# Kernel tuning notes

Hardware: AMD Instinct MI355X
Metric: run time of the kernel (lower is better)

Reference implementation:

```python
import jax, jax.numpy as jnp
import numpy as np

HIDDEN = 1024
HEADS = 16
HEAD_DIM = HIDDEN // HEADS
RANK = 256
B, S = 4, 2048


def setup_inputs() -> dict:
    key = jax.random.key(0)
    ks = jax.random.split(key, 10)
    sc_in = 1.0 / np.sqrt(HIDDEN)
    sc_r = 1.0 / np.sqrt(RANK)
    inp = {"hidden_states": jax.random.normal(ks[0], (B, S, HIDDEN), dtype=jnp.float32)}
    names = ["q", "k", "v"]
    for i, n in enumerate(names):
        inp[f"{n}A"] = jax.random.normal(ks[1 + 3 * i], (HIDDEN, RANK), dtype=jnp.float32) * sc_in
        inp[f"{n}B"] = jax.random.normal(ks[2 + 3 * i], (RANK, HIDDEN), dtype=jnp.float32) * sc_r
        inp[f"{n}b"] = jnp.zeros((HIDDEN,), dtype=jnp.float32)
    return inp


def _split_heads(x):
    # [B,S,H*D] -> [B,H,S,D]
    Bh, Sh, _ = x.shape
    return x.reshape(Bh, Sh, HEADS, HEAD_DIM).transpose(0, 2, 1, 3)


def reference(hidden_states, qA, qB, qb, kA, kB, kb, vA, vB, vb):
    # Low-rank projections: x @ A @ B + b (factorized linear)
    q = hidden_states @ qA @ qB + qb
    k = hidden_states @ kA @ kB + kb
    v = hidden_states @ vA @ vB + vb
    q = _split_heads(q)  # [B,H,S,D]
    k = _split_heads(k)
    v = _split_heads(v)
    scores = jnp.einsum("bhqd,bhkd->bhqk", q, k) / np.sqrt(HEAD_DIM)
    probs = jax.nn.softmax(scores, axis=-1)  # dropout is identity at inference
    ctx = jnp.einsum("bhqk,bhkd->bhqd", probs, v)
    ctx = ctx.transpose(0, 2, 1, 3).reshape(hidden_states.shape[0], hidden_states.shape[1], HIDDEN)
    return ctx
```

## Files before the change

kernel.cpp:

```cpp
#include <hip/hip_runtime.h>


typedef unsigned short u16;
typedef unsigned int   u32;
typedef __attribute__((ext_vector_type(4)))  float    f32x4;
typedef __attribute__((ext_vector_type(16))) float    f32x16;
typedef __attribute__((ext_vector_type(8)))  short    short8;
typedef __attribute__((ext_vector_type(8)))  _Float16 half8;
typedef __attribute__((ext_vector_type(4)))  u16      u16x4;

#define HID 1024
#define R_  256
#define S_  2048
#define B_  4
#define H_  16
#define D_  64
#define M_  (B_ * S_)

#define BM 128
#define BN 64
#define BK 64

#define KVB 64
#define NT  (S_ / KVB)
#define SCL 0.18033688011112f
#define MSHIFT 8.0f

__device__ __forceinline__ u16 f2h(float f) {
    _Float16 h = (_Float16)f;
    return __builtin_bit_cast(u16, h);
}
__device__ __forceinline__ u32 pkrtz(float a, float b) {
    auto r = __builtin_amdgcn_cvt_pkrtz(a, b);
    return __builtin_bit_cast(u32, r);
}

__device__ __forceinline__ f32x4 mfma16(short8 a, short8 b, f32x4 c) {
    return __builtin_amdgcn_mfma_f32_16x16x32_f16(
        __builtin_bit_cast(half8, a), __builtin_bit_cast(half8, b), c, 0, 0, 0);
}
__device__ __forceinline__ f32x16 mfma32(short8 a, short8 b, f32x16 c) {
    return __builtin_amdgcn_mfma_f32_32x32x16_f16(
        __builtin_bit_cast(half8, a), __builtin_bit_cast(half8, b), c, 0, 0, 0);
}

__device__ __forceinline__ void gload16(const u16* g, u16* l) {
    __builtin_amdgcn_global_load_lds(
        (__attribute__((address_space(1))) const void*)g,
        (__attribute__((address_space(3))) void*)l,
        16, 0, 0);
}

#if defined(__has_builtin)
#if __has_builtin(__builtin_amdgcn_permlane32_swap)
#define HAVE_PLSWAP 1
#endif
#endif
__device__ __forceinline__ void plswap(u32 x, u32 y, u32& lo, u32& hi) {
#ifdef HAVE_PLSWAP
    typedef __attribute__((ext_vector_type(2))) unsigned uv2;
    uv2 r = __builtin_amdgcn_permlane32_swap(x, y, false, false);
    lo = r.x; hi = r.y;
#else
    u32 ty = (u32)__shfl_xor((int)y, 32);
    u32 tx = (u32)__shfl_xor((int)x, 32);
    int h = (threadIdx.x & 63) >> 5;
    lo = h ? ty : x;
    hi = h ? y : tx;
#endif
}

__global__ __launch_bounds__(256) void prep_kernel(
    const float* __restrict__ hs, u16* __restrict__ hsb,
    const float* __restrict__ qA, const float* __restrict__ kA, const float* __restrict__ vA,
    const float* __restrict__ qB, const float* __restrict__ kB, const float* __restrict__ vB,
    u16* __restrict__ At, u16* __restrict__ Bt) {
    int bx = blockIdx.x;
    if (bx < 8192) {
        int i = (bx * 256 + threadIdx.x) * 4;
        float4 v = *(const float4*)(hs + i);
        u16x4 u;
        u[0] = f2h(v.x); u[1] = f2h(v.y); u[2] = f2h(v.z); u[3] = f2h(v.w);
        *(u16x4*)(hsb + i) = u;
        return;
    }
    int pb = bx - 8192;
    int which = pb >> 10;
    int o = (pb & 1023) * 256 + threadIdx.x;
    if (which < 3) {
        const float* src = (which == 0) ? qA : (which == 1) ? kA : vA;
        u16* dst = At + (size_t)which * R_ * HID;
        int c = o >> 10, r = o & 1023;
        dst[o] = f2h(src[(size_t)r * R_ + c]);
    } else {
        int w = which - 3;
        const float* src = (w == 0) ? qB : (w == 1) ? kB : vB;
        float scl = (w == 0) ? SCL : 1.0f;
        u16* dst = Bt + (size_t)w * HID * R_;
        int c = o >> 8, r = o & 255;
        dst[o] = f2h(src[(size_t)r * HID + c] * scl);
    }
}

template <int KDIM, int NOUT, bool QKV_OUT>
__global__ __launch_bounds__(256, 3) void gemm_kernel(
    const u16* __restrict__ X, const u16* __restrict__ Wt, u16* __restrict__ Y,
    u16* __restrict__ Yv,
    const float* __restrict__ bq, const float* __restrict__ bk, const float* __restrict__ bv) {
    const int w  = blockIdx.z;
    const int m0 = blockIdx.x * BM;
    const int n0 = blockIdx.y * BN;
    const u16* Xp = X + (QKV_OUT ? (size_t)w * M_ * KDIM : (size_t)0);
    const u16* Wp = Wt + (size_t)w * NOUT * KDIM;
    u16* Yp = Y + (size_t)w * M_ * NOUT;
    const float* bias = nullptr;
    float bscl = 1.0f;
    if constexpr (QKV_OUT) { bias = (w == 0) ? bq : (w == 1) ? bk : bv; bscl = (w == 0) ? SCL : 1.0f; }

    __shared__ __align__(16) u16 As[2][BM * BK];
    __shared__ __align__(16) u16 Bs[2][BN * BK];

    const int tid  = threadIdx.x;
    const int lane = tid & 63, wv = tid >> 6;
    const int l16 = lane & 15, lg = lane >> 4;
    const int wrow = (wv >> 1) * 64, wcol = (wv & 1) * 32;

    const int sr = lane >> 3, sp = lane & 7, sc = sp ^ sr;

#define G_STAGE(bf, k0)                                                       \
    {                                                                         \
        _Pragma("unroll")                                                     \
        for (int j = 0; j < 4; ++j) {                                         \
            int ra = wv * 32 + j * 8;                                         \
            gload16(Xp + (size_t)(m0 + ra + sr) * KDIM + (k0) + sc * 8,       \
                    &As[bf][ra * 64]);                                        \
        }                                                                     \
        _Pragma("unroll")                                                     \
        for (int j = 0; j < 2; ++j) {                                         \
            int rb = wv * 16 + j * 8;                                         \
            gload16(Wp + (size_t)(n0 + rb + sr) * KDIM + (k0) + sc * 8,       \
                    &Bs[bf][rb * 64]);                                        \
        }                                                                     \
    }

    f32x4 acc[4][2];
#pragma unroll
    for (int i = 0; i < 4; ++i)
#pragma unroll
        for (int j = 0; j < 2; ++j) acc[i][j] = (f32x4){0.f, 0.f, 0.f, 0.f};

    G_STAGE(0, 0);
    int cur = 0;
    for (int k0 = 0; k0 < KDIM; k0 += BK) {
        __syncthreads();
        if (k0 + BK < KDIM) G_STAGE(cur ^ 1, k0 + BK);
        const u16* ab = &As[cur][0];
        const u16* bb = &Bs[cur][0];
#pragma unroll
        for (int ks = 0; ks < 2; ++ks) {
            short8 af[4], bf[2];
#pragma unroll
            for (int ri = 0; ri < 4; ++ri) {
                int r = wrow + ri * 16 + l16;
                int c = ks * 4 + lg;
                af[ri] = *(const short8*)(ab + r * 64 + ((c ^ (r & 7)) * 8));
            }
#pragma unroll
            for (int ci = 0; ci < 2; ++ci) {
                int r = wcol + ci * 16 + l16;
                int c = ks * 4 + lg;
                bf[ci] = *(const short8*)(bb + r * 64 + ((c ^ (r & 7)) * 8));
            }
#pragma unroll
            for (int ri = 0; ri < 4; ++ri)
#pragma unroll
                for (int ci = 0; ci < 2; ++ci)
                    acc[ri][ci] = mfma16(af[ri], bf[ci], acc[ri][ci]);
        }
        cur ^= 1;
    }
#undef G_STAGE

    if constexpr (QKV_OUT) {
        if (w == 2) {
            const int bq_ = m0 >> 11;
            const int s_base = (m0 & 2047) + wrow + lg * 4;
#pragma unroll
            for (int ci = 0; ci < 2; ++ci) {
                int c = n0 + wcol + ci * 16 + l16;
                int h = c >> 6, d = c & 63;
                u16* colp = Yv + (((size_t)(bq_ * 16 + h) * 64 + d) << 11);
                float bi = bias[c];
#pragma unroll
                for (int ri = 0; ri < 4; ++ri)
#pragma unroll
                    for (int i = 0; i < 4; ++i)
                        colp[s_base + ri * 16 + i] = f2h(acc[ri][ci][i] + bi);
            }
            return;
        }
    }
#pragma unroll
    for (int ri = 0; ri < 4; ++ri)
#pragma unroll
        for (int ci = 0; ci < 2; ++ci)
#pragma unroll
            for (int i = 0; i < 4; ++i) {
                int r = m0 + wrow + ri * 16 + lg * 4 + i;
                int c = n0 + wcol + ci * 16 + l16;
                float val = acc[ri][ci][i];
                if constexpr (QKV_OUT) val += bias[c] * bscl;
                Yp[(size_t)r * NOUT + c] = f2h(val);
            }
}

__global__ __launch_bounds__(256, 2) void attn_kernel(
    const u16* __restrict__ Q, const u16* __restrict__ K,
    const u16* __restrict__ VT, float* __restrict__ out) {
    const int f = blockIdx.x;
    const int xcd = f & 7, idx = f >> 3;
    const int bh = xcd * 8 + (idx >> 3);
    const int qt = idx & 7;
    const int b = bh >> 4, h = bh & 15;
    const int tid = threadIdx.x, lane = tid & 63, wv = tid >> 6;
    const int l31 = lane & 31, hi = lane >> 5;
    const int q0 = qt * 256 + wv * 64;
    const int rx = l31 & 7;

    __shared__ __align__(16) u16 Ks[2][KVB * 64];
    __shared__ __align__(16) u16 Vs[2][KVB * 64];

    short8 qf0[4], qf1[4];
    {
        const u16* qp = Q + ((size_t)(b * S_ + q0 + l31)) * HID + h * D_ + 8 * hi;
        const u16* qp1 = qp + 32 * HID;
#pragma unroll
        for (int ks = 0; ks < 4; ++ks) {
            qf0[ks] = *(const short8*)(qp + 16 * ks);
            qf1[ks] = *(const short8*)(qp1 + 16 * ks);
        }
    }

    f32x16 ctx00, ctx01, ctx10, ctx11;
#pragma unroll
    for (int i = 0; i < 16; ++i) { ctx00[i] = 0.f; ctx01[i] = 0.f; ctx10[i] = 0.f; ctx11[i] = 0.f; }
    float la0 = 0.f, la1 = 0.f, la2 = 0.f, la3 = 0.f;
    float lb0 = 0.f, lb1 = 0.f, lb2 = 0.f, lb3 = 0.f;

    f32x16 minit;
#pragma unroll
    for (int i = 0; i < 16; ++i) minit[i] = -MSHIFT;
    asm volatile("" : "+v"(minit));

    const int r0p = tid >> 3, pos0 = tid & 7;
    const int rA = r0p, rB = r0p + 32;
    const int slA = pos0 ^ (rA & 7), slB = pos0 ^ (rB & 7);
    const size_t kofA = (size_t)rA * HID + slA * 8, kofB = (size_t)rB * HID + slB * 8;
    const size_t vofA = (size_t)rA * S_ + slA * 8,  vofB = (size_t)rB * S_ + slB * 8;
    const int wofA = rA * 64 + pos0 * 8, wofB = rB * 64 + pos0 * 8;

    const u16* Kcur = K + (size_t)(b * S_) * HID + h * D_;
    const u16* Vcur = VT + (size_t)bh * D_ * S_;

    short8 kst0, kst1, vst0, vst1;
    kst0 = *(const short8*)(Kcur + kofA);
    kst1 = *(const short8*)(Kcur + kofB);
    vst0 = *(const short8*)(Vcur + vofA);
    vst1 = *(const short8*)(Vcur + vofB);
    *(short8*)&Ks[0][wofA] = kst0;
    *(short8*)&Ks[0][wofB] = kst1;
    *(short8*)&Vs[0][wofA] = vst0;
    *(short8*)&Vs[0][wofB] = vst1;
    __syncthreads();

    for (int t = 0; t < NT; ++t) {
        const int buf = t & 1;
        if (t + 1 < NT) {
            const u16* Kn = Kcur + (size_t)(t + 1) * KVB * HID;
            const u16* Vn = Vcur + (size_t)(t + 1) * KVB;
            kst0 = *(const short8*)(Kn + kofA);
            kst1 = *(const short8*)(Kn + kofB);
            vst0 = *(const short8*)(Vn + vofA);
            vst1 = *(const short8*)(Vn + vofB);
        }

        f32x16 p00, p01, p10, p11;
        const u16* kb = &Ks[buf][0];
#pragma unroll
        for (int ks = 0; ks < 4; ++ks) {
            int sl = (2 * ks + hi) ^ rx;
            short8 a0 = *(const short8*)(kb + l31 * 64 + sl * 8);
            short8 a1 = *(const short8*)(kb + (32 + l31) * 64 + sl * 8);
            if (ks == 0) {
                p00 = mfma32(a0, qf0[0], minit);
                p01 = mfma32(a1, qf0[0], minit);
                p10 = mfma32(a0, qf1[0], minit);
                p11 = mfma32(a1, qf1[0], minit);
            } else {
                p00 = mfma32(a0, qf0[ks], p00);
                p01 = mfma32(a1, qf0[ks], p01);
                p10 = mfma32(a0, qf1[ks], p10);
                p11 = mfma32(a1, qf1[ks], p11);
            }
        }

#pragma unroll
        for (int i = 0; i < 16; ++i) {
            p00[i] = __builtin_amdgcn_exp2f(p00[i]);
            p01[i] = __builtin_amdgcn_exp2f(p01[i]);
            p10[i] = __builtin_amdgcn_exp2f(p10[i]);
            p11[i] = __builtin_amdgcn_exp2f(p11[i]);
        }
#pragma unroll
        for (int i = 0; i < 4; ++i) {
            la0 += p00[i] + p00[4 + i];
            la1 += p00[8 + i] + p00[12 + i];
            la2 += p01[i] + p01[4 + i];
            la3 += p01[8 + i] + p01[12 + i];
            lb0 += p10[i] + p10[4 + i];
            lb1 += p10[8 + i] + p10[12 + i];
            lb2 += p11[i] + p11[4 + i];
            lb3 += p11[8 + i] + p11[12 + i];
        }

        short8 pa0[4], pa1[4];
#define PACK_CHUNK(pv, base, dst)                                   \
        {                                                           \
            u32 x0 = pkrtz(pv[base + 0], pv[base + 1]);             \
            u32 x1 = pkrtz(pv[base + 2], pv[base + 3]);             \
            u32 x2 = pkrtz(pv[base + 4], pv[base + 5]);             \
            u32 x3 = pkrtz(pv[base + 6], pv[base + 7]);             \
            u32 w0, w1, w2, w3;                                     \
            plswap(x0, x2, w0, w2);                                 \
            plswap(x1, x3, w1, w3);                                 \
            union { u32 w[4]; short8 v; } uu;                       \
            uu.w[0] = w0; uu.w[1] = w1; uu.w[2] = w2; uu.w[3] = w3; \
            dst = uu.v;                                             \
        }
        PACK_CHUNK(p00, 0, pa0[0]);
        PACK_CHUNK(p00, 8, pa0[1]);
        PACK_CHUNK(p01, 0, pa0[2]);
        PACK_CHUNK(p01, 8, pa0[3]);
        PACK_CHUNK(p10, 0, pa1[0]);
        PACK_CHUNK(p10, 8, pa1[1]);
        PACK_CHUNK(p11, 0, pa1[2]);
        PACK_CHUNK(p11, 8, pa1[3]);
#undef PACK_CHUNK

        const u16* vb = &Vs[buf][0];
#pragma unroll
        for (int c = 0; c < 4; ++c) {
            int sl = (2 * c + hi) ^ rx;
            short8 v0 = *(const short8*)(vb + l31 * 64 + sl * 8);
            short8 v1 = *(const short8*)(vb + (32 + l31) * 64 + sl * 8);
            ctx00 = mfma32(v0, pa0[c], ctx00);
            ctx01 = mfma32(v1, pa0[c], ctx01);
            ctx10 = mfma32(v0, pa1[c], ctx10);
            ctx11 = mfma32(v1, pa1[c], ctx11);
        }

        __syncthreads();
        if (t + 1 < NT) {
            const int nb = 1 - buf;
            *(short8*)&Ks[nb][wofA] = kst0;
            *(short8*)&Ks[nb][wofB] = kst1;
            *(short8*)&Vs[nb][wofA] = vst0;
            *(short8*)&Vs[nb][wofB] = vst1;
        }
        __syncthreads();
    }

    float l0 = (la0 + la1) + (la2 + la3);
    l0 += __shfl_xor(l0, 32);
    float l1 = (lb0 + lb1) + (lb2 + lb3);
    l1 += __shfl_xor(l1, 32);
    float invl0 = 1.0f / l0, invl1 = 1.0f / l1;
    float* op0 = out + ((size_t)(b * S_ + q0 + l31)) * HID + h * D_;
    float* op1 = op0 + (size_t)32 * HID;
#pragma unroll
    for (int g = 0; g < 4; ++g) {
        f32x4 o00, o01, o10, o11;
#pragma unroll
        for (int i = 0; i < 4; ++i) {
            o00[i] = ctx00[4 * g + i] * invl0;
            o01[i] = ctx01[4 * g + i] * invl0;
            o10[i] = ctx10[4 * g + i] * invl1;
            o11[i] = ctx11[4 * g + i] * invl1;
        }
        *(f32x4*)(op0 + 8 * g + 4 * hi) = o00;
        *(f32x4*)(op0 + 32 + 8 * g + 4 * hi) = o01;
        *(f32x4*)(op1 + 8 * g + 4 * hi) = o10;
        *(f32x4*)(op1 + 32 + 8 * g + 4 * hi) = o11;
    }
}

extern "C" void kernel_launch(void* const* d_in, const int* in_sizes, int n_in,
                              void* d_out, int out_size, void* d_ws, size_t ws_size,
                              hipStream_t stream) {
    const float* hs = (const float*)d_in[0];
    const float* qA = (const float*)d_in[1];
    const float* qB = (const float*)d_in[2];
    const float* qb = (const float*)d_in[3];
    const float* kA = (const float*)d_in[4];
    const float* kB = (const float*)d_in[5];
    const float* kb = (const float*)d_in[6];
    const float* vA = (const float*)d_in[7];
    const float* vB = (const float*)d_in[8];
    const float* vb = (const float*)d_in[9];

    char* ws = (char*)d_ws;
    size_t off = 0;
    u16* hsb = (u16*)(ws + off); off += (size_t)M_ * HID * 2;
    u16* At  = (u16*)(ws + off); off += (size_t)3 * R_ * HID * 2;
    u16* Bt  = (u16*)(ws + off); off += (size_t)3 * HID * R_ * 2;
    u16* T   = (u16*)(ws + off); off += (size_t)3 * M_ * R_ * 2;
    u16* QKV = (u16*)(ws + off); off += (size_t)3 * M_ * HID * 2;
    u16* VT  = (u16*)(ws + off);

    prep_kernel<<<dim3(8192 + 6144), 256, 0, stream>>>(hs, hsb, qA, kA, vA, qB, kB, vB, At, Bt);

    gemm_kernel<HID, R_, false><<<dim3(M_ / BM, R_ / BN, 3), 256, 0, stream>>>(
        hsb, At, T, nullptr, nullptr, nullptr, nullptr);
    gemm_kernel<R_, HID, true><<<dim3(M_ / BM, HID / BN, 3), 256, 0, stream>>>(
        T, Bt, QKV, VT, qb, kb, vb);

    attn_kernel<<<dim3(512), 256, 0, stream>>>(
        QKV, QKV + (size_t)M_ * HID, VT, (float*)d_out);
}
```

Before: 143.4 us.

## Load K/V fragments directly from global into registers, dropping LDS staging

Replaces the double-buffered shared-memory K/V tiles and the two barriers per iteration with per-wave register fragments loaded straight from global memory in MFMA operand layout. The next tile's K is prefetched after the QK MFMAs and V after the PV MFMAs. This removes LDS traffic and block-wide synchronisation. In exchange, each of the four waves fetches the same KV data from global/L2 separately, and register pressure rises.

```diff
diff --git a/kernel.cpp b/kernel.cpp
--- a/kernel.cpp
+++ b/kernel.cpp
@@ -225,10 +225,6 @@
     const int tid = threadIdx.x, lane = tid & 63, wv = tid >> 6;
     const int l31 = lane & 31, hi = lane >> 5;
     const int q0 = qt * 256 + wv * 64;
-    const int rx = l31 & 7;
-
-    __shared__ __align__(16) u16 Ks[2][KVB * 64];
-    __shared__ __align__(16) u16 Vs[2][KVB * 64];
 
     short8 qf0[4], qf1[4];
     {
@@ -252,45 +248,39 @@
     for (int i = 0; i < 16; ++i) minit[i] = -MSHIFT;
     asm volatile("" : "+v"(minit));
 
-    const int r0p = tid >> 3, pos0 = tid & 7;
-    const int rA = r0p, rB = r0p + 32;
-    const int slA = pos0 ^ (rA & 7), slB = pos0 ^ (rB & 7);
-    const size_t kofA = (size_t)rA * HID + slA * 8, kofB = (size_t)rB * HID + slB * 8;
-    const size_t vofA = (size_t)rA * S_ + slA * 8,  vofB = (size_t)rB * S_ + slB * 8;
-    const int wofA = rA * 64 + pos0 * 8, wofB = rB * 64 + pos0 * 8;
-
-    const u16* Kcur = K + (size_t)(b * S_) * HID + h * D_;
-    const u16* Vcur = VT + (size_t)bh * D_ * S_;
-
-    short8 kst0, kst1, vst0, vst1;
-    kst0 = *(const short8*)(Kcur + kofA);
-    kst1 = *(const short8*)(Kcur + kofB);
-    vst0 = *(const short8*)(Vcur + vofA);
-    vst1 = *(const short8*)(Vcur + vofB);
-    *(short8*)&Ks[0][wofA] = kst0;
-    *(short8*)&Ks[0][wofB] = kst1;
-    *(short8*)&Vs[0][wofA] = vst0;
-    *(short8*)&Vs[0][wofB] = vst1;
-    __syncthreads();
+    const u16* Kb = K + ((size_t)(b * S_ + l31)) * HID + h * D_ + 8 * hi;
+    const u16* Vb = VT + ((size_t)bh * D_ + l31) * S_ + 8 * hi;
+
+    short8 kf[8], vf[8];
+#define LOAD_K(kv0)                                                           \
+    {                                                                         \
+        const u16* kp = Kb + (size_t)(kv0) * HID;                             \
+        _Pragma("unroll")                                                     \
+        for (int j = 0; j < 4; ++j) {                                         \
+            kf[j]     = *(const short8*)(kp + 16 * j);                        \
+            kf[4 + j] = *(const short8*)(kp + (size_t)32 * HID + 16 * j);     \
+        }                                                                     \
+    }
+#define LOAD_V(kv0)                                                           \
+    {                                                                         \
+        const u16* vp = Vb + (kv0);                                           \
+        _Pragma("unroll")                                                     \
+        for (int j = 0; j < 4; ++j) {                                         \
+            vf[j]     = *(const short8*)(vp + 16 * j);                        \
+            vf[4 + j] = *(const short8*)(vp + (size_t)32 * S_ + 16 * j);      \
+        }                                                                     \
+    }
+
+    LOAD_K(0);
+    LOAD_V(0);
 
     for (int t = 0; t < NT; ++t) {
-        const int buf = t & 1;
-        if (t + 1 < NT) {
-            const u16* Kn = Kcur + (size_t)(t + 1) * KVB * HID;
-            const u16* Vn = Vcur + (size_t)(t + 1) * KVB;
-            kst0 = *(const short8*)(Kn + kofA);
-            kst1 = *(const short8*)(Kn + kofB);
-            vst0 = *(const short8*)(Vn + vofA);
-            vst1 = *(const short8*)(Vn + vofB);
-        }
+        const bool more = (t + 1 < NT);
 
         f32x16 p00, p01, p10, p11;
-        const u16* kb = &Ks[buf][0];
 #pragma unroll
         for (int ks = 0; ks < 4; ++ks) {
-            int sl = (2 * ks + hi) ^ rx;
-            short8 a0 = *(const short8*)(kb + l31 * 64 + sl * 8);
-            short8 a1 = *(const short8*)(kb + (32 + l31) * 64 + sl * 8);
+            short8 a0 = kf[ks], a1 = kf[4 + ks];
             if (ks == 0) {
                 p00 = mfma32(a0, qf0[0], minit);
                 p01 = mfma32(a1, qf0[0], minit);
@@ -303,6 +293,7 @@
                 p11 = mfma32(a1, qf1[ks], p11);
             }
         }
+        if (more) LOAD_K((t + 1) * KVB);
 
 #pragma unroll
         for (int i = 0; i < 16; ++i) {
@@ -347,28 +338,18 @@
         PACK_CHUNK(p11, 8, pa1[3]);
 #undef PACK_CHUNK
 
-        const u16* vb = &Vs[buf][0];
 #pragma unroll
         for (int c = 0; c < 4; ++c) {
-            int sl = (2 * c + hi) ^ rx;
-            short8 v0 = *(const short8*)(vb + l31 * 64 + sl * 8);
-            short8 v1 = *(const short8*)(vb + (32 + l31) * 64 + sl * 8);
+            short8 v0 = vf[c], v1 = vf[4 + c];
             ctx00 = mfma32(v0, pa0[c], ctx00);
             ctx01 = mfma32(v1, pa0[c], ctx01);
             ctx10 = mfma32(v0, pa1[c], ctx10);
             ctx11 = mfma32(v1, pa1[c], ctx11);
         }
-
-        __syncthreads();
-        if (t + 1 < NT) {
-            const int nb = 1 - buf;
-            *(short8*)&Ks[nb][wofA] = kst0;
-            *(short8*)&Ks[nb][wofB] = kst1;
-            *(short8*)&Vs[nb][wofA] = vst0;
-            *(short8*)&Vs[nb][wofB] = vst1;
-        }
-        __syncthreads();
-    }
+        if (more) LOAD_V((t + 1) * KVB);
+    }
+#undef LOAD_K
+#undef LOAD_V
 
     float l0 = (la0 + la1) + (la2 + la3);
     l0 += __shfl_xor(l0, 32);
```

Result: slower. 244.3 us (+70.3%).

## Halve attention block to two waves and drop redundant barrier

Applied to the files above, without the earlier changes.

The attention kernel now uses 128-thread blocks that each cover 128 query rows, with twice as many blocks so more workgroups can be resident per CU. Each thread stages four K rows and four V rows per tile instead of two. The barrier before writing the next double-buffer slot is removed, leaving one barrier per KV tile; this is safe because every wave has already passed the previous iteration's barrier. The cost is that K/V tiles are loaded from L2 twice as often overall, since each block serves fewer queries.

```diff
diff --git a/kernel.cpp b/kernel.cpp
--- a/kernel.cpp
+++ b/kernel.cpp
@@ -214,18 +214,17 @@
             }
 }
 
-__global__ __launch_bounds__(256, 2) void attn_kernel(
+__global__ __launch_bounds__(128, 2) void attn_kernel(
     const u16* __restrict__ Q, const u16* __restrict__ K,
     const u16* __restrict__ VT, float* __restrict__ out) {
     const int f = blockIdx.x;
     const int xcd = f & 7, idx = f >> 3;
-    const int bh = xcd * 8 + (idx >> 3);
-    const int qt = idx & 7;
+    const int bh = xcd * 8 + (idx >> 4);
+    const int qt = idx & 15;
     const int b = bh >> 4, h = bh & 15;
     const int tid = threadIdx.x, lane = tid & 63, wv = tid >> 6;
     const int l31 = lane & 31, hi = lane >> 5;
-    const int q0 = qt * 256 + wv * 64;
-    const int rx = l31 & 7;
+    const int q0 = qt * 128 + wv * 64;
 
     __shared__ __align__(16) u16 Ks[2][KVB * 64];
     __shared__ __align__(16) u16 Vs[2][KVB * 64];
@@ -252,36 +251,47 @@
     for (int i = 0; i < 16; ++i) minit[i] = -MSHIFT;
     asm volatile("" : "+v"(minit));
 
+    const int rx = l31 & 7;
+
     const int r0p = tid >> 3, pos0 = tid & 7;
-    const int rA = r0p, rB = r0p + 32;
-    const int slA = pos0 ^ (rA & 7), slB = pos0 ^ (rB & 7);
-    const size_t kofA = (size_t)rA * HID + slA * 8, kofB = (size_t)rB * HID + slB * 8;
-    const size_t vofA = (size_t)rA * S_ + slA * 8,  vofB = (size_t)rB * S_ + slB * 8;
-    const int wofA = rA * 64 + pos0 * 8, wofB = rB * 64 + pos0 * 8;
+    const int sl0 = pos0 ^ (r0p & 7);
+    size_t kof[4], vof[4];
+    int wof[4];
+#pragma unroll
+    for (int p = 0; p < 4; ++p) {
+        int r = r0p + 16 * p;
+        kof[p] = (size_t)r * HID + sl0 * 8;
+        vof[p] = (size_t)r * S_ + sl0 * 8;
+        wof[p] = r * 64 + pos0 * 8;
+    }
 
     const u16* Kcur = K + (size_t)(b * S_) * HID + h * D_;
     const u16* Vcur = VT + (size_t)bh * D_ * S_;
 
-    short8 kst0, kst1, vst0, vst1;
-    kst0 = *(const short8*)(Kcur + kofA);
-    kst1 = *(const short8*)(Kcur + kofB);
-    vst0 = *(const short8*)(Vcur + vofA);
-    vst1 = *(const short8*)(Vcur + vofB);
-    *(short8*)&Ks[0][wofA] = kst0;
-    *(short8*)&Ks[0][wofB] = kst1;
-    *(short8*)&Vs[0][wofA] = vst0;
-    *(short8*)&Vs[0][wofB] = vst1;
+    short8 kst[4], vst[4];
+#pragma unroll
+    for (int p = 0; p < 4; ++p) {
+        kst[p] = *(const short8*)(Kcur + kof[p]);
+        vst[p] = *(const short8*)(Vcur + vof[p]);
+    }
+#pragma unroll
+    for (int p = 0; p < 4; ++p) {
+        *(short8*)&Ks[0][wof[p]] = kst[p];
+        *(short8*)&Vs[0][wof[p]] = vst[p];
+    }
     __syncthreads();
 
     for (int t = 0; t < NT; ++t) {
         const int buf = t & 1;
-        if (t + 1 < NT) {
+        const bool more = (t + 1 < NT);
+        if (more) {
             const u16* Kn = Kcur + (size_t)(t + 1) * KVB * HID;
             const u16* Vn = Vcur + (size_t)(t + 1) * KVB;
-            kst0 = *(const short8*)(Kn + kofA);
-            kst1 = *(const short8*)(Kn + kofB);
-            vst0 = *(const short8*)(Vn + vofA);
-            vst1 = *(const short8*)(Vn + vofB);
+#pragma unroll
+            for (int p = 0; p < 4; ++p) {
+                kst[p] = *(const short8*)(Kn + kof[p]);
+                vst[p] = *(const short8*)(Vn + vof[p]);
+            }
         }
 
         f32x16 p00, p01, p10, p11;
@@ -359,15 +369,15 @@
             ctx11 = mfma32(v1, pa1[c], ctx11);
         }
 
-        __syncthreads();
-        if (t + 1 < NT) {
+        if (more) {
             const int nb = 1 - buf;
-            *(short8*)&Ks[nb][wofA] = kst0;
-            *(short8*)&Ks[nb][wofB] = kst1;
-            *(short8*)&Vs[nb][wofA] = vst0;
-            *(short8*)&Vs[nb][wofB] = vst1;
-        }
-        __syncthreads();
+#pragma unroll
+            for (int p = 0; p < 4; ++p) {
+                *(short8*)&Ks[nb][wof[p]] = kst[p];
+                *(short8*)&Vs[nb][wof[p]] = vst[p];
+            }
+            __syncthreads();
+        }
     }
 
     float l0 = (la0 + la1) + (la2 + la3);
@@ -424,6 +434,6 @@
     gemm_kernel<R_, HID, true><<<dim3(M_ / BM, HID / BN, 3), 256, 0, stream>>>(
         T, Bt, QKV, VT, qb, kb, vb);
 
-    attn_kernel<<<dim3(512), 256, 0, stream>>>(
+    attn_kernel<<<dim3(1024), 128, 0, stream>>>(
         QKV, QKV + (size_t)M_ * HID, VT, (float*)d_out);
 }
```

New measurement: 151.2 us. 5.5% more time.
